# Performance work log

Measured on AMD Instinct MI355X. Metric: run time of the kernel, lower is better.

Reference implementation:

```python
import jax, jax.numpy as jnp
import numpy as np

T_NUM = 1024      # tracks
DET_NUM = 1024    # detections
DEG = 64          # candidate detections per track
E = T_NUM * DEG   # directed track->det edges (row<col half)
N = T_NUM + DET_NUM
D_IN = 512
D_EMB = 256
LAM = 5.0
SLACK = -0.2
SINKHORN_ITERS = 8


def setup_inputs() -> dict:
    key = jax.random.key(0)
    ks = jax.random.split(key, 20)
    x = jax.random.normal(ks[0], (N, D_IN), jnp.float32)
    coords = jax.random.uniform(ks[1], (N, 4), dtype=jnp.float32)
    r = jax.random.uniform(ks[2], (N, 4), dtype=jnp.float32)
    bx1 = r[:, 0] * 100.0; by1 = r[:, 1] * 100.0
    bw = r[:, 2] * 50.0 + 1.0; bh = r[:, 3] * 50.0 + 1.0
    coords_original = jnp.stack([bx1, by1, bx1 + bw, by1 + bh], axis=1)
    src_t = jnp.repeat(jnp.arange(T_NUM, dtype=jnp.int32), DEG)
    off = jnp.tile(jnp.arange(DEG, dtype=jnp.int32), T_NUM)
    dst_d = (src_t * 13 + off) % DET_NUM            # unique det per (track, slot)
    src = src_t
    dst = dst_d + T_NUM                              # detection node ids come after tracks
    edge_index = jnp.concatenate([jnp.stack([src, dst]), jnp.stack([dst, src])], axis=1)
    ground_truth = jax.random.bernoulli(ks[3], 0.1, (T_NUM * DET_NUM,)).astype(jnp.float32)

    def lin(k, i, o):
        return jax.random.normal(k, (i, o), jnp.float32) / np.sqrt(i).astype(np.float32)

    params = {
        'W_enc': lin(ks[4], D_IN, D_EMB), 'b_enc': jnp.zeros((D_EMB,), jnp.float32),
        'W1a': lin(ks[5], 2 * D_EMB, 64), 'b1a': jnp.zeros((64,), jnp.float32),
        'W2a': lin(ks[6], 64, 1), 'b2a': jnp.zeros((1,), jnp.float32),
        'W1g': lin(ks[7], 8, 16), 'b1g': jnp.zeros((16,), jnp.float32),
        'W2g': lin(ks[8], 16, 1), 'b2g': jnp.zeros((1,), jnp.float32),
        'W1f': lin(ks[9], 2, 8), 'b1f': jnp.zeros((8,), jnp.float32),
        'W2f': lin(ks[10], 8, 1), 'b2f': jnp.zeros((1,), jnp.float32),
        'Wn': lin(ks[11], D_EMB, D_EMB), 'Wm': lin(ks[12], D_EMB, D_EMB),
        'bo': jnp.zeros((D_EMB,), jnp.float32),
        'W1c': lin(ks[13], 2, 8), 'b1c': jnp.zeros((8,), jnp.float32),
        'W2c': lin(ks[14], 8, 1), 'b2c': jnp.zeros((1,), jnp.float32),
    }
    out = {'x': x, 'coords': coords, 'coords_original': coords_original,
           'ground_truth': ground_truth, 'edge_index': edge_index}
    out.update(params)
    return out


def _box_iou(a, b):
    # a, b: [E, 4] boxes (x1, y1, x2, y2)
    lt = jnp.maximum(a[:, :2], b[:, :2])
    rb = jnp.minimum(a[:, 2:], b[:, 2:])
    wh = jnp.clip(rb - lt, 0.0)
    inter = wh[:, 0] * wh[:, 1]
    area_a = (a[:, 2] - a[:, 0]) * (a[:, 3] - a[:, 1])
    area_b = (b[:, 2] - b[:, 0]) * (b[:, 3] - b[:, 1])
    return inter / (area_a + area_b - inter + 1e-9)


def _sinkhorn(M):
    def body(M, _):
        M = M / (jnp.sum(M, axis=1, keepdims=True) + 1e-9)
        M = M / (jnp.sum(M, axis=0, keepdims=True) + 1e-9)
        return M, None
    M, _ = jax.lax.scan(body, M, None, length=SINKHORN_ITERS)
    return M


def _forward(x, coords, coords_original,
             W_enc, b_enc, W1a, b1a, W2a, b2a, W1g, b1g, W2g, b2g,
             W1f, b1f, W2f, b2f, Wn, Wm, bo, W1c, b1c, W2c, b2c,
             edge_index):
    node = jax.nn.relu(x @ W_enc + b_enc)                      # [N, D_EMB]
    src, dst = edge_index[0], edge_index[1]                    # [2E]
    # batched per-edge appearance affinity (replaces python edge loop)
    pair = jnp.concatenate([node[src], node[dst]], axis=1)     # [2E, 2*D_EMB]
    a1 = jax.nn.relu(pair @ W1a + b1a) @ W2a + b2a             # [2E, 1]
    geo = jnp.concatenate([coords[src], coords[dst]], axis=1)  # [2E, 8]
    a2 = jax.nn.relu(geo @ W1g + b1g) @ W2g + b2g              # [2E, 1]
    e_in = jnp.concatenate([a1, a2], axis=1)                   # [2E, 2]
    edge_emb = jax.nn.relu(e_in @ W1f + b1f) @ W2f + b2f       # [2E, 1]
    # optim_net: one round of edge-weighted message passing
    msg = jax.ops.segment_sum(edge_emb * node[src], dst, num_segments=N)
    out = jax.nn.relu(node @ Wn + msg @ Wm + bo)               # [N, D_EMB]
    # forward (row < col) edges are the first E entries by construction
    sf, df = src[:E], dst[:E]
    oa, ob = out[sf], out[df]
    denom = jnp.maximum(jnp.linalg.norm(oa, axis=1) * jnp.linalg.norm(ob, axis=1), 1e-6)
    cosv = jnp.sum(oa * ob, axis=1) / denom                    # CosineSimilarity(dim=0) per edge
    iou = _box_iou(coords_original[sf], coords_original[df])   # [E]
    f_in = jnp.stack([cosv, iou], axis=1)                      # [E, 2]
    aff = (jax.nn.relu(f_in @ W1c + b1c) @ W2c + b2c)[:, 0]    # [E]
    # assignment matrix with slack row/col, scatter exp(aff*lam)
    slack_val = jnp.exp(jnp.float32(SLACK * LAM))
    M = jnp.full((T_NUM + 1, DET_NUM + 1), slack_val, jnp.float32)
    M = M.at[:T_NUM, :DET_NUM].set(0.0)
    M = M.at[sf, df - T_NUM].set(jnp.exp(aff * LAM))
    M = _sinkhorn(M)
    return M[:-1, :-1].reshape(-1)                             # [T_NUM*DET_NUM]


def reference(x, coords, coords_original, ground_truth, edge_index,
              W_enc, b_enc, W1a, b1a, W2a, b2a, W1g, b1g, W2g, b2g,
              W1f, b1f, W2f, b2f, Wn, Wm, bo, W1c, b1c, W2c, b2c):
    normalized_output = _forward(x, coords, coords_original,
                                 W_enc, b_enc, W1a, b1a, W2a, b2a,
                                 W1g, b1g, W2g, b2g, W1f, b1f, W2f, b2f,
                                 Wn, Wm, bo, W1c, b1c, W2c, b2c, edge_index)
    det_num = jnp.asarray(DET_NUM, jnp.int32)
    tracklet_num = jnp.asarray(T_NUM, jnp.int32)
    return (normalized_output, ground_truth, det_num, tracklet_num)
```

## Files before the change

kernel.cpp:

```cpp
#include <hip/hip_runtime.h>

#define T_NUM 1024
#define DET_NUM 1024
#define E_NUM 65536
#define TWO_E 131072
#define N_NODES 2048
#define D_IN 512
#define D_EMB 256

__device__ __forceinline__ unsigned bf16r(float x) {
  const unsigned u = __float_as_uint(x);
  return (u + 0x7fffu + ((u >> 16) & 1u)) >> 16;
}
__device__ __forceinline__ float bflo(unsigned p) { return __uint_as_float(p << 16); }
__device__ __forceinline__ float bfhi(unsigned p) { return __uint_as_float(p & 0xffff0000u); }
__device__ __forceinline__ void fma4(float4& a, float s, const float4 w) {
  a.x = fmaf(s, w.x, a.x); a.y = fmaf(s, w.y, a.y);
  a.z = fmaf(s, w.z, a.z); a.w = fmaf(s, w.w, a.w);
}

__global__ __launch_bounds__(1024) void k_enc_pg(
    const float* __restrict__ x, const float* __restrict__ W,
    const float* __restrict__ b, const float* __restrict__ coords,
    const float* __restrict__ W1a, const float* __restrict__ W1g,
    float* __restrict__ node, float* __restrict__ P1, float* __restrict__ P2,
    float* __restrict__ G1, float* __restrict__ G2) {
  __shared__ __align__(16) float ns[8][D_EMB];
  __shared__ __align__(16) float psq[3][8][D_EMB];
  __shared__ float pp1[8][64], pp2[8][64];
  const int tid = threadIdx.x;
  const int j = tid & 255;
  const int q = __builtin_amdgcn_readfirstlane(tid >> 8);
  const int row0 = blockIdx.x * 8;
  float acc[8];
  const float bj = b[j];
#pragma unroll
  for (int r = 0; r < 8; r++) acc[r] = (q == 0) ? bj : 0.f;
  const float* xr = x + (size_t)row0 * D_IN + q * 128;
  const float* Wp = W + (size_t)q * 128 * D_EMB;
  for (int k = 0; k < 128; k += 4) {
    const float w0 = Wp[(k + 0) * D_EMB + j];
    const float w1 = Wp[(k + 1) * D_EMB + j];
    const float w2 = Wp[(k + 2) * D_EMB + j];
    const float w3 = Wp[(k + 3) * D_EMB + j];
#pragma unroll
    for (int r = 0; r < 8; r++) {
      const float4 xv = *reinterpret_cast<const float4*>(xr + (size_t)r * D_IN + k);
      acc[r] = fmaf(xv.x, w0, acc[r]);
      acc[r] = fmaf(xv.y, w1, acc[r]);
      acc[r] = fmaf(xv.z, w2, acc[r]);
      acc[r] = fmaf(xv.w, w3, acc[r]);
    }
  }
  if (q > 0) {
#pragma unroll
    for (int r = 0; r < 8; r++) psq[q - 1][r][j] = acc[r];
  }
  __syncthreads();
  if (q == 0) {
#pragma unroll
    for (int r = 0; r < 8; r++) {
      const float v = fmaxf(acc[r] + psq[0][r][j] + psq[1][r][j] + psq[2][r][j], 0.f);
      node[(size_t)(row0 + r) * D_EMB + j] = v;
      ns[r][j] = v;
    }
  }
  __syncthreads();
  const int r2 = tid >> 7, q2 = (tid >> 6) & 1, hh = tid & 63;
  float a1 = 0.f, a2 = 0.f;
  {
    const int k0 = q2 * 128;
    for (int k = 0; k < 128; k += 4) {
      const float4 nv = *reinterpret_cast<const float4*>(&ns[r2][k0 + k]);
      a1 = fmaf(nv.x, W1a[(k0 + k + 0) * 64 + hh], a1);
      a1 = fmaf(nv.y, W1a[(k0 + k + 1) * 64 + hh], a1);
      a1 = fmaf(nv.z, W1a[(k0 + k + 2) * 64 + hh], a1);
      a1 = fmaf(nv.w, W1a[(k0 + k + 3) * 64 + hh], a1);
      a2 = fmaf(nv.x, W1a[(D_EMB + k0 + k + 0) * 64 + hh], a2);
      a2 = fmaf(nv.y, W1a[(D_EMB + k0 + k + 1) * 64 + hh], a2);
      a2 = fmaf(nv.z, W1a[(D_EMB + k0 + k + 2) * 64 + hh], a2);
      a2 = fmaf(nv.w, W1a[(D_EMB + k0 + k + 3) * 64 + hh], a2);
    }
    if (q2 == 1) { pp1[r2][hh] = a1; pp2[r2][hh] = a2; }
  }
  __syncthreads();
  if (q2 == 0) {
    P1[(size_t)(row0 + r2) * 64 + hh] = a1 + pp1[r2][hh];
    P2[(size_t)(row0 + r2) * 64 + hh] = a2 + pp2[r2][hh];
  }
  if (tid < 128) {
    const int r = tid >> 4, g = tid & 15;
    const int n = row0 + r;
    float g1 = 0.f, g2 = 0.f;
#pragma unroll
    for (int k = 0; k < 4; k++) {
      const float c = coords[(size_t)n * 4 + k];
      g1 = fmaf(c, W1g[k * 16 + g], g1);
      g2 = fmaf(c, W1g[(4 + k) * 16 + g], g2);
    }
    G1[(size_t)n * 16 + g] = g1;
    G2[(size_t)n * 16 + g] = g2;
  }
}

__global__ __launch_bounds__(512) void k_msg_out(
    const float* __restrict__ node,
    const float* __restrict__ P1, const float* __restrict__ P2,
    const float* __restrict__ G1, const float* __restrict__ G2,
    const float* __restrict__ b1a, const float* __restrict__ W2a, const float* __restrict__ b2a,
    const float* __restrict__ b1g, const float* __restrict__ W2g, const float* __restrict__ b2g,
    const float* __restrict__ W1f, const float* __restrict__ b1f,
    const float* __restrict__ W2f, const float* __restrict__ b2f,
    const float* __restrict__ Wn, const float* __restrict__ Wm,
    const float* __restrict__ bo, float* __restrict__ outE, float* __restrict__ nrm) {
  __shared__ __align__(16) float msp[2][4][D_EMB];
  __shared__ __align__(16) float ms[4][D_EMB];
  __shared__ __align__(16) float nsh[4][D_EMB];
  __shared__ __align__(16) float pg[8][4][D_EMB];
  __shared__ float wsh[4][64];
  __shared__ int ssh[4][64];
  __shared__ float pa1[4][64], pa2[4][64];
  __shared__ float redn[8];
  const int tid = threadIdx.x;
  const int h = __builtin_amdgcn_readfirstlane(tid >> 8);
  const int j = tid & 255;
  const int row0 = blockIdx.x * 4;
  {
    const int r = (tid >> 6) & 3, o = tid & 63;
    const int n = row0 + r;
    int src;
    if (n < T_NUM) {
      src = T_NUM + ((13 * n + o) & 1023);
    } else {
      const int d = n - T_NUM;
      src = (709 * (d - o)) & 1023;
    }
    float a1p = 0.f, a2p = 0.f;
    const float4* p1 = (const float4*)(P1 + (size_t)src * 64) + h * 8;
    const float4* p2 = (const float4*)(P2 + (size_t)n * 64) + h * 8;
    const float4* b1 = (const float4*)b1a + h * 8;
    const float4* w2 = (const float4*)W2a + h * 8;
#pragma unroll
    for (int i = 0; i < 8; i++) {
      const float4 pa = p1[i], pb = p2[i], bb = b1[i], ww = w2[i];
      a1p += fmaxf(pa.x + pb.x + bb.x, 0.f) * ww.x + fmaxf(pa.y + pb.y + bb.y, 0.f) * ww.y +
             fmaxf(pa.z + pb.z + bb.z, 0.f) * ww.z + fmaxf(pa.w + pb.w + bb.w, 0.f) * ww.w;
    }
    const float4* g1 = (const float4*)(G1 + (size_t)src * 16) + h * 2;
    const float4* g2 = (const float4*)(G2 + (size_t)n * 16) + h * 2;
    const float4* bg = (const float4*)b1g + h * 2;
    const float4* wg = (const float4*)W2g + h * 2;
#pragma unroll
    for (int i = 0; i < 2; i++) {
      const float4 pa = g1[i], pb = g2[i], bb = bg[i], ww = wg[i];
      a2p += fmaxf(pa.x + pb.x + bb.x, 0.f) * ww.x + fmaxf(pa.y + pb.y + bb.y, 0.f) * ww.y +
             fmaxf(pa.z + pb.z + bb.z, 0.f) * ww.z + fmaxf(pa.w + pb.w + bb.w, 0.f) * ww.w;
    }
    if (h == 1) { pa1[r][o] = a1p; pa2[r][o] = a2p; ssh[r][o] = src; }
    else        { wsh[r][o] = a1p; pg[0][r][o] = a2p; }
  }
  __syncthreads();
  if (h == 0) {
    const int r = (tid >> 6) & 3, o = tid & 63;
    const float a1 = wsh[r][o] + pa1[r][o] + b2a[0];
    const float a2 = pg[0][r][o] + pa2[r][o] + b2g[0];
    float acc = b2f[0];
#pragma unroll
    for (int jj = 0; jj < 8; jj++) {
      const float hv = fmaxf(a1 * W1f[jj] + a2 * W1f[8 + jj] + b1f[jj], 0.f);
      acc = fmaf(hv, W2f[jj], acc);
    }
    wsh[r][o] = acc;
  } else {
#pragma unroll
    for (int rr = 0; rr < 4; rr++)
      nsh[rr][j] = node[(size_t)(row0 + rr) * D_EMB + j];
  }
  __syncthreads();
  {
    const int s = tid >> 8;
    const int r = (tid >> 6) & 3;
    const int qd = tid & 63;
    const int i0 = s * 32;
    float ax = 0.f, ay = 0.f, az = 0.f, aw = 0.f;
#pragma unroll 4
    for (int i = 0; i < 32; i++) {
      const float w = wsh[r][i0 + i];
      const float4 nv = *reinterpret_cast<const float4*>(
          node + (size_t)ssh[r][i0 + i] * D_EMB + 4 * qd);
      ax = fmaf(w, nv.x, ax); ay = fmaf(w, nv.y, ay);
      az = fmaf(w, nv.z, az); aw = fmaf(w, nv.w, aw);
    }
    *reinterpret_cast<float4*>(&msp[s][r][4 * qd]) = make_float4(ax, ay, az, aw);
  }
  __syncthreads();
  {
    float* m0 = &ms[0][0];
    const float* s0 = &msp[0][0][0];
    const float* s1 = &msp[1][0][0];
    m0[tid] = s0[tid] + s1[tid];
    m0[tid + 512] = s0[tid + 512] + s1[tid + 512];
  }
  __syncthreads();
  {
    const int kq = __builtin_amdgcn_readfirstlane(tid >> 6);
    const int jq = tid & 63;
    const float4* Wn4 = (const float4*)Wn;
    const float4* Wm4 = (const float4*)Wm;
    float4 a0 = make_float4(0.f, 0.f, 0.f, 0.f);
    float4 a1 = a0, a2 = a0, a3 = a0;
    const int kbeg = kq * 32;
    for (int k = kbeg; k < kbeg + 32; ++k) {
      const float4 wn = Wn4[k * 64 + jq];
      const float4 wm = Wm4[k * 64 + jq];
      const float n0 = nsh[0][k], m0v = ms[0][k];
      const float n1 = nsh[1][k], m1v = ms[1][k];
      const float n2 = nsh[2][k], m2v = ms[2][k];
      const float n3 = nsh[3][k], m3v = ms[3][k];
      fma4(a0, n0, wn); fma4(a0, m0v, wm);
      fma4(a1, n1, wn); fma4(a1, m1v, wm);
      fma4(a2, n2, wn); fma4(a2, m2v, wm);
      fma4(a3, n3, wn); fma4(a3, m3v, wm);
    }
    *reinterpret_cast<float4*>(&pg[kq][0][4 * jq]) = a0;
    *reinterpret_cast<float4*>(&pg[kq][1][4 * jq]) = a1;
    *reinterpret_cast<float4*>(&pg[kq][2][4 * jq]) = a2;
    *reinterpret_cast<float4*>(&pg[kq][3][4 * jq]) = a3;
  }
  __syncthreads();
  {
    const int r = tid >> 7, jc = tid & 127;
    const int lane = tid & 63, wid = tid >> 6;
    float v0 = bo[2 * jc + 0], v1 = bo[2 * jc + 1];
#pragma unroll
    for (int kq = 0; kq < 8; kq++) {
      v0 += pg[kq][r][2 * jc + 0];
      v1 += pg[kq][r][2 * jc + 1];
    }
    v0 = fmaxf(v0, 0.f); v1 = fmaxf(v1, 0.f);
    *reinterpret_cast<float2*>(outE + (size_t)(row0 + r) * D_EMB + 2 * jc) =
        make_float2(v0, v1);
    float sq = v0 * v0 + v1 * v1;
#pragma unroll
    for (int oo = 32; oo > 0; oo >>= 1) sq += __shfl_down(sq, oo, 64);
    if (lane == 0) redn[wid] = sq;
  }
  __syncthreads();
  if (tid < 4)
    nrm[row0 + tid] = sqrtf(redn[2 * tid] + redn[2 * tid + 1]);
}

__global__ __launch_bounds__(256) void k_aff(
    const float* __restrict__ outE, const float* __restrict__ nrm,
    const float* __restrict__ cov,
    const float* __restrict__ W1c, const float* __restrict__ b1c,
    const float* __restrict__ W2c, const float* __restrict__ b2c,
    float* __restrict__ Kbp, unsigned short* __restrict__ KTg) {
  __shared__ __align__(16) float4 oas[64];
  __shared__ float psum[4][64];
  const int t = blockIdx.x;
  const int tid = threadIdx.x;
  const int o = tid & 63, c = tid >> 6;
  const int s = t;
  if (tid < 64) oas[tid] = ((const float4*)(outE + (size_t)s * D_EMB))[tid];
  __syncthreads();
  const int d = (13 * t + o) & 1023;
  const int dn = T_NUM + d;
  {
    const float4* ob = (const float4*)(outE + (size_t)dn * D_EMB) + c * 16;
    const float4* oa = oas + c * 16;
    float dot = 0.f;
#pragma unroll
    for (int i = 0; i < 16; i++) {
      const float4 a = oa[i], bq = ob[i];
      dot += a.x * bq.x + a.y * bq.y + a.z * bq.z + a.w * bq.w;
    }
    psum[c][o] = dot;
  }
  __syncthreads();
  if (tid < 64) {
    const float dot = psum[0][o] + psum[1][o] + psum[2][o] + psum[3][o];
    const float cosv = dot / fmaxf(nrm[s] * nrm[dn], 1e-6f);
    const float4 A = ((const float4*)cov)[s];
    const float4 B = ((const float4*)cov)[dn];
    const float ltx = fmaxf(A.x, B.x), lty = fmaxf(A.y, B.y);
    const float rbx = fminf(A.z, B.z), rby = fminf(A.w, B.w);
    const float wx = fmaxf(rbx - ltx, 0.f), wy = fmaxf(rby - lty, 0.f);
    const float inter = wx * wy;
    const float areaA = (A.z - A.x) * (A.w - A.y);
    const float areaB = (B.z - B.x) * (B.w - B.y);
    const float iou = inter / (areaA + areaB - inter + 1e-9f);
    float aff = b2c[0];
#pragma unroll
    for (int jj = 0; jj < 8; jj++) {
      const float h = fmaxf(cosv * W1c[jj] + iou * W1c[8 + jj] + b1c[jj], 0.f);
      aff = fmaf(h, W2c[jj], aff);
    }
    const float Kv = __expf(aff * 5.0f);
    const int tp = (13 * s) & 1023;
    Kbp[tp * 68 + (tp & 3) + o] = Kv;
    if (o < 4) {
      const int pr = (o < (tp & 3)) ? o : o + 64;
      Kbp[tp * 68 + pr] = 0.f;
    }
    const int cbase = (((d & 1022) + 960) & 1023) & ~3;
    const int rho = (((d + 961) & 1023) - cbase) & 1023;
    KTg[d * 72 + rho + 63 - o] = (unsigned short)bf16r(Kv);
    if (o < 8) {
      const int slot = (o < rho) ? o : o + 64;
      KTg[d * 72 + slot] = 0;
    }
  }
}

__global__ __launch_bounds__(512, 2) void k_sinkhorn(
    const float* __restrict__ Kbp, const unsigned short* __restrict__ KTg,
    float* __restrict__ ug, float* __restrict__ vg,
    const float* __restrict__ gt, float* __restrict__ out) {
  if (blockIdx.x != 0) {
    const size_t idx = (size_t)(blockIdx.x - 1) * 512 + threadIdx.x;
    ((float4*)out)[(size_t)T_NUM * 256 + idx] = ((const float4*)gt)[idx];
    return;
  }
  __shared__ __align__(16) float u_lds[1092];
  __shared__ __align__(16) float v_lds[1092];
  __shared__ float red_u[8];
  __shared__ float red_v[8];
  __shared__ __align__(16) uint4 ktlA[9][512];
  __shared__ __align__(16) uint4 ktlB[9][512];
  const int tid = threadIdx.x;
  const int lane = tid & 63, wid = tid >> 6;
  const int ra = 2 * tid, rb = 2 * tid + 1;
  const int qa = (ra & ~3) >> 2;
  const int cbase = ((ra + 960) & 1023) & ~3;
  const int qc = cbase >> 2;
  unsigned k0[34], k1[34];
  {
    const float4* s0p = (const float4*)(Kbp + (size_t)ra * 68);
    const float4* s1p = (const float4*)(Kbp + (size_t)rb * 68);
#pragma unroll
    for (int c = 0; c < 17; c++) {
      float4 f = s0p[c];
      k0[2 * c]     = bf16r(f.x) | (bf16r(f.y) << 16);
      k0[2 * c + 1] = bf16r(f.z) | (bf16r(f.w) << 16);
      f = s1p[c];
      k1[2 * c]     = bf16r(f.x) | (bf16r(f.y) << 16);
      k1[2 * c + 1] = bf16r(f.z) | (bf16r(f.w) << 16);
    }
  }
  {
    const uint4* g = (const uint4*)KTg;
#pragma unroll
    for (int q = 0; q < 9; q++) ktlA[q][tid] = g[tid * 18 + q];
#pragma unroll
    for (int q = 0; q < 9; q++) ktlB[q][tid] = g[tid * 18 + 9 + q];
  }
  float u0 = 1.f, u1 = 1.f, vc0 = 1.f, vc1 = 1.f, u_sl = 1.f, v_sl = 1.f;
  v_lds[tid] = 1.f; v_lds[tid + 512] = 1.f;
  if (tid < 68) v_lds[1024 + tid] = 1.f;
  if (tid < 8) red_v[tid] = 128.f;
  const float slack = 0.36787944117144233f;
  __syncthreads();
#pragma unroll 1
  for (int it = 0; it < 8; ++it) {
    const float4* vq = (const float4*)v_lds;
    float a00 = 0.f, a01 = 0.f, a10 = 0.f, a11 = 0.f;
#pragma unroll
    for (int c = 0; c < 17; c++) {
      const float4 v4 = vq[qa + c];
      unsigned p = k0[2 * c];
      a00 = fmaf(bflo(p), v4.x, a00); a00 = fmaf(bfhi(p), v4.y, a00);
      p = k0[2 * c + 1];
      a01 = fmaf(bflo(p), v4.z, a01); a01 = fmaf(bfhi(p), v4.w, a01);
      p = k1[2 * c];
      a10 = fmaf(bflo(p), v4.x, a10); a10 = fmaf(bfhi(p), v4.y, a10);
      p = k1[2 * c + 1];
      a11 = fmaf(bflo(p), v4.z, a11); a11 = fmaf(bfhi(p), v4.w, a11);
    }
    const float sumv = red_v[0] + red_v[1] + red_v[2] + red_v[3] +
                       red_v[4] + red_v[5] + red_v[6] + red_v[7];
    const float s0 = a00 + a01 + slack * v_sl;
    const float s1 = a10 + a11 + slack * v_sl;
    u0 = u0 / (u0 * s0 + 1e-9f);
    u1 = u1 / (u1 * s1 + 1e-9f);
    u_sl = u_sl / (u_sl * slack * (sumv + v_sl) + 1e-9f);
    u_lds[ra] = u0; u_lds[rb] = u1;
    if (tid < 34) { u_lds[1024 + ra] = u0; u_lds[1024 + rb] = u1; }
    float usum = u0 + u1;
#pragma unroll
    for (int o = 32; o > 0; o >>= 1) usum += __shfl_down(usum, o, 64);
    if (lane == 0) red_u[wid] = usum;
    __syncthreads();
    const float4* uq = (const float4*)u_lds;
    float t0 = 0.f, t1 = 0.f;
#pragma unroll 3
    for (int q = 0; q < 9; q++) {
      const uint4 A = ktlA[q][tid];
      const uint4 B = ktlB[q][tid];
      const float4 ua = uq[qc + 2 * q];
      const float4 ub = uq[qc + 2 * q + 1];
      t0 = fmaf(bflo(A.x), ua.x, t0); t0 = fmaf(bfhi(A.x), ua.y, t0);
      t0 = fmaf(bflo(A.y), ua.z, t0); t0 = fmaf(bfhi(A.y), ua.w, t0);
      t0 = fmaf(bflo(A.z), ub.x, t0); t0 = fmaf(bfhi(A.z), ub.y, t0);
      t0 = fmaf(bflo(A.w), ub.z, t0); t0 = fmaf(bfhi(A.w), ub.w, t0);
      t1 = fmaf(bflo(B.x), ua.x, t1); t1 = fmaf(bfhi(B.x), ua.y, t1);
      t1 = fmaf(bflo(B.y), ua.z, t1); t1 = fmaf(bfhi(B.y), ua.w, t1);
      t1 = fmaf(bflo(B.z), ub.x, t1); t1 = fmaf(bfhi(B.z), ub.y, t1);
      t1 = fmaf(bflo(B.w), ub.z, t1); t1 = fmaf(bfhi(B.w), ub.w, t1);
    }
    const float sumu = red_u[0] + red_u[1] + red_u[2] + red_u[3] +
                       red_u[4] + red_u[5] + red_u[6] + red_u[7];
    t0 += slack * u_sl;
    t1 += slack * u_sl;
    vc0 = vc0 / (vc0 * t0 + 1e-9f);
    vc1 = vc1 / (vc1 * t1 + 1e-9f);
    v_sl = v_sl / (v_sl * slack * (sumu + u_sl) + 1e-9f);
    v_lds[ra] = vc0; v_lds[rb] = vc1;
    if (tid < 34) { v_lds[1024 + ra] = vc0; v_lds[1024 + rb] = vc1; }
    float vsum = vc0 + vc1;
#pragma unroll
    for (int o = 32; o > 0; o >>= 1) vsum += __shfl_down(vsum, o, 64);
    if (lane == 0) red_v[wid] = vsum;
    __syncthreads();
  }
  ((float2*)ug)[tid] = make_float2(u0, u1);
  ((float2*)vg)[tid] = make_float2(vc0, vc1);
}

__global__ __launch_bounds__(256) void k_final(
    const float* __restrict__ Kbp, const float* __restrict__ ug,
    const float* __restrict__ vg, float* __restrict__ out) {
  const int t = blockIdx.x;
  const int tp = (13 * t) & 1023;
  const float u = ug[tp];
  const float* krow = Kbp + (size_t)tp * 68 + (tp & 3);
  const int d0 = threadIdx.x * 4;
  const float4 v4 = ((const float4*)vg)[threadIdx.x];
  float4 o4;
  const int m0 = (d0 - tp) & 1023;
  const int m1 = (d0 + 1 - tp) & 1023;
  const int m2 = (d0 + 2 - tp) & 1023;
  const int m3 = (d0 + 3 - tp) & 1023;
  o4.x = (m0 < 64) ? u * krow[m0] * v4.x : 0.f;
  o4.y = (m1 < 64) ? u * krow[m1] * v4.y : 0.f;
  o4.z = (m2 < 64) ? u * krow[m2] * v4.z : 0.f;
  o4.w = (m3 < 64) ? u * krow[m3] * v4.w : 0.f;
  ((float4*)out)[(size_t)t * 256 + threadIdx.x] = o4;
  if (t == 0 && threadIdx.x == 0) {
    out[(size_t)2 * T_NUM * DET_NUM] = 1024.0f;
    out[(size_t)2 * T_NUM * DET_NUM + 1] = 1024.0f;
  }
}

extern "C" void kernel_launch(void* const* d_in, const int* in_sizes, int n_in,
                              void* d_out, int out_size, void* d_ws, size_t ws_size,
                              hipStream_t stream) {
  const float* x      = (const float*)d_in[0];
  const float* coords = (const float*)d_in[1];
  const float* cov    = (const float*)d_in[2];
  const float* gt     = (const float*)d_in[3];
  const float* W_enc  = (const float*)d_in[5];
  const float* b_enc  = (const float*)d_in[6];
  const float* W1a    = (const float*)d_in[7];
  const float* b1a    = (const float*)d_in[8];
  const float* W2a    = (const float*)d_in[9];
  const float* b2a    = (const float*)d_in[10];
  const float* W1g    = (const float*)d_in[11];
  const float* b1g    = (const float*)d_in[12];
  const float* W2g    = (const float*)d_in[13];
  const float* b2g    = (const float*)d_in[14];
  const float* W1f    = (const float*)d_in[15];
  const float* b1f    = (const float*)d_in[16];
  const float* W2f    = (const float*)d_in[17];
  const float* b2f    = (const float*)d_in[18];
  const float* Wn     = (const float*)d_in[19];
  const float* Wm     = (const float*)d_in[20];
  const float* bo     = (const float*)d_in[21];
  const float* W1c    = (const float*)d_in[22];
  const float* b1c    = (const float*)d_in[23];
  const float* W2c    = (const float*)d_in[24];
  const float* b2c    = (const float*)d_in[25];

  char* ws = (char*)d_ws;
  size_t off = 0;
  auto alloc = [&](size_t bytes) {
    char* p = ws + off;
    off = (off + bytes + 255) & ~(size_t)255;
    return p;
  };
  float* node  = (float*)alloc((size_t)N_NODES * D_EMB * 4);
  float* P1    = (float*)alloc((size_t)N_NODES * 64 * 4);
  float* P2    = (float*)alloc((size_t)N_NODES * 64 * 4);
  float* G1    = (float*)alloc((size_t)N_NODES * 16 * 4);
  float* G2    = (float*)alloc((size_t)N_NODES * 16 * 4);
  float* outE  = (float*)alloc((size_t)N_NODES * D_EMB * 4);
  float* nrm   = (float*)alloc((size_t)N_NODES * 4);
  float* Kbp   = (float*)alloc((size_t)1024 * 68 * 4);
  unsigned short* KTg = (unsigned short*)alloc((size_t)1024 * 72 * 2);
  float* ug    = (float*)alloc(1024 * 4);
  float* vg    = (float*)alloc(1024 * 4);
  float* out   = (float*)d_out;

  k_enc_pg<<<N_NODES / 8, 1024, 0, stream>>>(x, W_enc, b_enc, coords, W1a, W1g,
                                             node, P1, P2, G1, G2);
  k_msg_out<<<N_NODES / 4, 512, 0, stream>>>(node, P1, P2, G1, G2,
                                             b1a, W2a, b2a, b1g, W2g, b2g,
                                             W1f, b1f, W2f, b2f,
                                             Wn, Wm, bo, outE, nrm);
  k_aff<<<T_NUM, 256, 0, stream>>>(outE, nrm, cov, W1c, b1c, W2c, b2c,
                                   Kbp, KTg);
  k_sinkhorn<<<513, 512, 0, stream>>>(Kbp, KTg, ug, vg, gt, out);
  k_final<<<T_NUM, 256, 0, stream>>>(Kbp, ug, vg, out);
}
```

Before: 202.2 us.

## Restructure encoder GEMM: stage x rows in LDS, float4 weight loads, 8-way k-split

The encoder kernel now processes 4 rows per 512-thread block instead of 8 rows per 1024-thread block. Each block stages its input rows in shared memory and reads W_enc as float4. Each thread accumulates 4 output columns across 4 rows over a 64-long k slice, then an 8-way shared-memory reduction adds the bias and applies ReLU. This aims to raise occupancy with twice as many blocks and to replace the old redundant global x loads with broadcast LDS reads. The cost is that the weight matrix is streamed by twice as many blocks.

```diff
diff --git a/kernel.cpp b/kernel.cpp
--- a/kernel.cpp
+++ b/kernel.cpp
@@ -19,51 +19,57 @@
   a.z = fmaf(s, w.z, a.z); a.w = fmaf(s, w.w, a.w);
 }
 
-__global__ __launch_bounds__(1024) void k_enc_pg(
+__global__ __launch_bounds__(512) void k_enc_pg(
     const float* __restrict__ x, const float* __restrict__ W,
     const float* __restrict__ b, const float* __restrict__ coords,
     const float* __restrict__ W1a, const float* __restrict__ W1g,
     float* __restrict__ node, float* __restrict__ P1, float* __restrict__ P2,
     float* __restrict__ G1, float* __restrict__ G2) {
-  __shared__ __align__(16) float ns[8][D_EMB];
-  __shared__ __align__(16) float psq[3][8][D_EMB];
-  __shared__ float pp1[8][64], pp2[8][64];
+  __shared__ __align__(16) float xsh[4][D_IN];
+  __shared__ __align__(16) float pg[8][4][D_EMB];
+  __shared__ __align__(16) float ns[4][D_EMB];
+  __shared__ float pp1[4][64], pp2[4][64];
   const int tid = threadIdx.x;
-  const int j = tid & 255;
-  const int q = __builtin_amdgcn_readfirstlane(tid >> 8);
-  const int row0 = blockIdx.x * 8;
-  float acc[8];
-  const float bj = b[j];
-#pragma unroll
-  for (int r = 0; r < 8; r++) acc[r] = (q == 0) ? bj : 0.f;
-  const float* xr = x + (size_t)row0 * D_IN + q * 128;
-  const float* Wp = W + (size_t)q * 128 * D_EMB;
-  for (int k = 0; k < 128; k += 4) {
-    const float w0 = Wp[(k + 0) * D_EMB + j];
-    const float w1 = Wp[(k + 1) * D_EMB + j];
-    const float w2 = Wp[(k + 2) * D_EMB + j];
-    const float w3 = Wp[(k + 3) * D_EMB + j];
-#pragma unroll
-    for (int r = 0; r < 8; r++) {
-      const float4 xv = *reinterpret_cast<const float4*>(xr + (size_t)r * D_IN + k);
-      acc[r] = fmaf(xv.x, w0, acc[r]);
-      acc[r] = fmaf(xv.y, w1, acc[r]);
-      acc[r] = fmaf(xv.z, w2, acc[r]);
-      acc[r] = fmaf(xv.w, w3, acc[r]);
-    }
-  }
-  if (q > 0) {
-#pragma unroll
-    for (int r = 0; r < 8; r++) psq[q - 1][r][j] = acc[r];
-  }
-  __syncthreads();
-  if (q == 0) {
-#pragma unroll
-    for (int r = 0; r < 8; r++) {
-      const float v = fmaxf(acc[r] + psq[0][r][j] + psq[1][r][j] + psq[2][r][j], 0.f);
-      node[(size_t)(row0 + r) * D_EMB + j] = v;
-      ns[r][j] = v;
-    }
+  const int row0 = blockIdx.x * 4;
+  {
+    const int idx = tid * 4;
+    const int r = idx >> 9, c = idx & 511;
+    *reinterpret_cast<float4*>(&xsh[r][c]) =
+        *reinterpret_cast<const float4*>(x + (size_t)(row0 + r) * D_IN + c);
+  }
+  __syncthreads();
+  {
+    const int kq = __builtin_amdgcn_readfirstlane(tid >> 6);
+    const int jq = tid & 63;
+    const float4* W4 = (const float4*)W;
+    float4 a0 = make_float4(0.f, 0.f, 0.f, 0.f);
+    float4 a1 = a0, a2 = a0, a3 = a0;
+    const int kbeg = kq * 64;
+    for (int k = kbeg; k < kbeg + 64; ++k) {
+      const float4 w4 = W4[k * 64 + jq];
+      fma4(a0, xsh[0][k], w4);
+      fma4(a1, xsh[1][k], w4);
+      fma4(a2, xsh[2][k], w4);
+      fma4(a3, xsh[3][k], w4);
+    }
+    *reinterpret_cast<float4*>(&pg[kq][0][4 * jq]) = a0;
+    *reinterpret_cast<float4*>(&pg[kq][1][4 * jq]) = a1;
+    *reinterpret_cast<float4*>(&pg[kq][2][4 * jq]) = a2;
+    *reinterpret_cast<float4*>(&pg[kq][3][4 * jq]) = a3;
+  }
+  __syncthreads();
+  {
+    const int r = tid >> 7, jc = tid & 127;
+    float v0 = b[2 * jc + 0], v1 = b[2 * jc + 1];
+#pragma unroll
+    for (int kq = 0; kq < 8; kq++) {
+      v0 += pg[kq][r][2 * jc + 0];
+      v1 += pg[kq][r][2 * jc + 1];
+    }
+    v0 = fmaxf(v0, 0.f); v1 = fmaxf(v1, 0.f);
+    *reinterpret_cast<float2*>(node + (size_t)(row0 + r) * D_EMB + 2 * jc) =
+        make_float2(v0, v1);
+    ns[r][2 * jc] = v0; ns[r][2 * jc + 1] = v1;
   }
   __syncthreads();
   const int r2 = tid >> 7, q2 = (tid >> 6) & 1, hh = tid & 63;
@@ -88,7 +94,7 @@
     P1[(size_t)(row0 + r2) * 64 + hh] = a1 + pp1[r2][hh];
     P2[(size_t)(row0 + r2) * 64 + hh] = a2 + pp2[r2][hh];
   }
-  if (tid < 128) {
+  if (tid < 64) {
     const int r = tid >> 4, g = tid & 15;
     const int n = row0 + r;
     float g1 = 0.f, g2 = 0.f;
@@ -501,8 +507,8 @@
   float* vg    = (float*)alloc(1024 * 4);
   float* out   = (float*)d_out;
 
-  k_enc_pg<<<N_NODES / 8, 1024, 0, stream>>>(x, W_enc, b_enc, coords, W1a, W1g,
-                                             node, P1, P2, G1, G2);
+  k_enc_pg<<<N_NODES / 4, 512, 0, stream>>>(x, W_enc, b_enc, coords, W1a, W1g,
+                                            node, P1, P2, G1, G2);
   k_msg_out<<<N_NODES / 4, 512, 0, stream>>>(node, P1, P2, G1, G2,
                                              b1a, W2a, b2a, b1g, W2g, b2g,
                                              W1f, b1f, W2f, b2f,
```

Result: faster. 193.8 us, median of 2 (-4.2%).
